# Optimization experiments

Measured on AMD Instinct MI355X. Metric: run time of the kernel, lower is better.

## Reference

```python
import jax, jax.numpy as jnp
import numpy as np

DIM = 768
HEADS = 12
HEAD_DIM = 64
INNER = HEADS * HEAD_DIM  # 768


def setup_inputs() -> dict:
    key = jax.random.key(0)
    k_x, k_wqkv, k_bqkv, k_wout, k_bout = jax.random.split(key, 5)
    B, S = 2, 2048
    x = jax.random.normal(k_x, (B, S, DIM), dtype=jnp.float32)
    # nn.Linear(dim, 3*inner): weight [out, in]; store transposed for x @ W
    lim = 1.0 / np.sqrt(DIM)
    w_qkv = jax.random.uniform(k_wqkv, (DIM, 3 * INNER), minval=-lim, maxval=lim, dtype=jnp.float32)
    b_qkv = jax.random.uniform(k_bqkv, (3 * INNER,), minval=-lim, maxval=lim, dtype=jnp.float32)
    lim2 = 1.0 / np.sqrt(INNER)
    # original zero-inits to_out; use random weights so the reference output is non-trivial
    w_out = jax.random.uniform(k_wout, (INNER, DIM), minval=-lim2, maxval=lim2, dtype=jnp.float32)
    b_out = jax.random.uniform(k_bout, (DIM,), minval=-lim2, maxval=lim2, dtype=jnp.float32)
    return {"x": x, "w_qkv": w_qkv, "b_qkv": b_qkv, "w_out": w_out, "b_out": b_out}


def reference(x, w_qkv, b_qkv, w_out, b_out):
    B, S, _ = x.shape
    qkv = x @ w_qkv + b_qkv                               # [B, S, 3*H*D]
    qkv = qkv.reshape(B, S, 3, HEADS, HEAD_DIM)           # b s three h d
    q, k, v = qkv[:, :, 0], qkv[:, :, 1], qkv[:, :, 2]    # each [B, S, H, D]
    scale = 1.0 / np.sqrt(HEAD_DIM)
    # non-causal self-attention (FlashSelfAttention, dropout=0, causal=False)
    scores = jnp.einsum('bshd,bthd->bhst', q, k) * scale  # [B, H, S, S]
    attn = jax.nn.softmax(scores, axis=-1)
    ctx = jnp.einsum('bhst,bthd->bshd', attn, v)          # [B, S, H, D]
    ctx = ctx.reshape(B, S, INNER)
    return ctx @ w_out + b_out                            # [B, S, DIM]
```

## Files before the change

kernel.cpp:

```cpp
#include <hip/hip_runtime.h>
#include <cstddef>
#include <cstdint>

#define DIM  768
#define NH   12
#define HD   64
#define SEQ  2048
#define NB   2
#define NQKV 2304
#define G    (NB * NH * SEQ)

typedef _Float16 f16x8 __attribute__((ext_vector_type(8)));
typedef _Float16 f16x4 __attribute__((ext_vector_type(4)));
typedef float    f32x4 __attribute__((ext_vector_type(4)));
typedef float    f32x16 __attribute__((ext_vector_type(16)));

#if __has_builtin(__builtin_amdgcn_exp2f)
#define EXP2(x) __builtin_amdgcn_exp2f(x)
#else
#define EXP2(x) exp2f(x)
#endif

#define QSCALE 0.1803368801111244f
#define C2     6.0f

__device__ __forceinline__ void gld16(const _Float16* g, _Float16* l) {
  __builtin_amdgcn_global_load_lds(
      (const __attribute__((address_space(1))) void*)g,
      (__attribute__((address_space(3))) void*)l, 16, 0, 0);
}

__global__ __launch_bounds__(256) void cvt_f16_kernel(
    const float* __restrict__ in, _Float16* __restrict__ out) {
  const size_t i = ((size_t)blockIdx.x * 256 + threadIdx.x) * 8;
  float4 f0 = *(const float4*)(in + i), f1 = *(const float4*)(in + i + 4);
  f16x8 o;
  o[0] = (_Float16)f0.x; o[1] = (_Float16)f0.y; o[2] = (_Float16)f0.z; o[3] = (_Float16)f0.w;
  o[4] = (_Float16)f1.x; o[5] = (_Float16)f1.y; o[6] = (_Float16)f1.z; o[7] = (_Float16)f1.w;
  *(f16x8*)(out + i) = o;
}

__global__ __launch_bounds__(256) void transpose_cvt_kernel(
    const float* __restrict__ W, _Float16* __restrict__ WT, int K, int N) {
  __shared__ _Float16 tl[32][36];
  const int t = threadIdx.x;
  const int k0 = blockIdx.y * 32, n0 = blockIdx.x * 32;
  {
    const int r = t >> 3, c4 = (t & 7) * 4;
    float4 f = *(const float4*)(W + (size_t)(k0 + r) * N + n0 + c4);
    tl[r][c4 + 0] = (_Float16)f.x; tl[r][c4 + 1] = (_Float16)f.y;
    tl[r][c4 + 2] = (_Float16)f.z; tl[r][c4 + 3] = (_Float16)f.w;
  }
  __syncthreads();
  const int n = t >> 3, kc = (t & 7) * 4;
  f16x4 v;
  v[0] = tl[kc + 0][n]; v[1] = tl[kc + 1][n];
  v[2] = tl[kc + 2][n]; v[3] = tl[kc + 3][n];
  *(f16x4*)(WT + (size_t)(n0 + n) * K + k0 + kc) = v;
}

__global__ __launch_bounds__(256) void vtrans_kernel(
    const _Float16* __restrict__ v, _Float16* __restrict__ vT) {
  __shared__ _Float16 tl[64][68];
  const int t = threadIdx.x;
  const int bh = blockIdx.x, st = blockIdx.y;
  const size_t base = (size_t)bh * SEQ * HD;
  {
    const int s = t >> 2, dc = (t & 3) * 16;
    const _Float16* p = v + base + (size_t)(st * 64 + s) * HD + dc;
    f16x8 a = *(const f16x8*)p, b = *(const f16x8*)(p + 8);
    *(f16x8*)&tl[s][dc] = a;
    *(f16x8*)&tl[s][dc + 8] = b;
  }
  __syncthreads();
  const int d = t >> 2, sc = (t & 3) * 16;
  f16x8 o0, o1;
#pragma unroll
  for (int j = 0; j < 8; j++) { o0[j] = tl[sc + j][d]; o1[j] = tl[sc + 8 + j][d]; }
  _Float16* q = vT + base + (size_t)d * SEQ + st * 64 + sc;
  *(f16x8*)q = o0;
  *(f16x8*)(q + 8) = o1;
}

template <int SC>
__global__ __launch_bounds__(256) void gemm_f16_kernel(
    const _Float16* __restrict__ A, const _Float16* __restrict__ BT,
    const float* __restrict__ bias, void* __restrict__ p0,
    void* __restrict__ p1, void* __restrict__ p2, int M, int N, int K) {
  __shared__ _Float16 As[128 * 32];
  __shared__ _Float16 Bs[128 * 32];
  const int tid = threadIdx.x;
  const int lane = tid & 63, wv = tid >> 6;
  const int wm = wv >> 1, wn = wv & 1;
  const int quad = lane >> 4, lcol = lane & 15;
  const int bm = blockIdx.y * 128, bn = blockIdx.x * 128;

  f32x4 acc[4][4];
#pragma unroll
  for (int i = 0; i < 4; i++)
#pragma unroll
    for (int j = 0; j < 4; j++) acc[i][j] = (f32x4)(0.f);

  const int r0 = wv * 32 + (lane >> 2);
  const int kp = (((lane & 3) ^ ((r0 >> 1) & 3)) * 8);
  const _Float16* a0p = A + (size_t)(bm + r0) * K + kp;
  const _Float16* a1p = A + (size_t)(bm + r0 + 16) * K + kp;
  const _Float16* b0p = BT + (size_t)(bn + r0) * K + kp;
  const _Float16* b1p = BT + (size_t)(bn + r0 + 16) * K + kp;
  _Float16* lA0 = As + (wv * 2 + 0) * 512;
  _Float16* lA1 = As + (wv * 2 + 1) * 512;
  _Float16* lB0 = Bs + (wv * 2 + 0) * 512;
  _Float16* lB1 = Bs + (wv * 2 + 1) * 512;

  for (int k0 = 0; k0 < K; k0 += 32) {
    __syncthreads();
    gld16(a0p + k0, lA0);
    gld16(a1p + k0, lA1);
    gld16(b0p + k0, lB0);
    gld16(b1p + k0, lB1);
    __syncthreads();

    f16x8 af[4], bf[4];
#pragma unroll
    for (int mi = 0; mi < 4; mi++) {
      const int R = wm * 64 + mi * 16 + lcol;
      af[mi] = *(const f16x8*)&As[R * 32 + (quad ^ ((R >> 1) & 3)) * 8];
    }
#pragma unroll
    for (int ni = 0; ni < 4; ni++) {
      const int R = wn * 64 + ni * 16 + lcol;
      bf[ni] = *(const f16x8*)&Bs[R * 32 + (quad ^ ((R >> 1) & 3)) * 8];
    }
#pragma unroll
    for (int mi = 0; mi < 4; mi++)
#pragma unroll
      for (int ni = 0; ni < 4; ni++)
        acc[mi][ni] = __builtin_amdgcn_mfma_f32_16x16x32_f16(af[mi], bf[ni], acc[mi][ni], 0, 0, 0);
  }

#pragma unroll
  for (int mi = 0; mi < 4; mi++) {
#pragma unroll
    for (int r = 0; r < 4; r++) {
      const int row = bm + wm * 64 + mi * 16 + quad * 4 + r;
      const int b_ = row >> 11, s_ = row & 2047;
#pragma unroll
      for (int ni = 0; ni < 4; ni++) {
        const int c = bn + wn * 64 + ni * 16 + lcol;
        const float val = acc[mi][ni][r] + bias[c];
        if (!SC) {
          ((float*)p0)[(size_t)row * N + c] = val;
        } else {
          const int d = c & 63;
          const int which = c / 768;
          const int h = (c - which * 768) >> 6;
          const size_t idx = (((size_t)b_ * NH + h) * SEQ + s_) * HD + d;
          if (which == 0)      ((_Float16*)p0)[idx] = (_Float16)(val * QSCALE);
          else if (which == 1) ((_Float16*)p1)[idx] = (_Float16)val;
          else                 ((_Float16*)p2)[idx] = (_Float16)val;
        }
      }
    }
  }
}

#define PST 68
__global__ __launch_bounds__(256) void attn_part_kernel(
    const _Float16* __restrict__ Q, const _Float16* __restrict__ K,
    const _Float16* __restrict__ V, _Float16* __restrict__ Ohat,
    float* __restrict__ L) {
  __shared__ _Float16 Ks[64 * PST];
  __shared__ _Float16 Vs[64 * PST];
  __shared__ _Float16 Ps[128 * PST];
  const int tid = threadIdx.x, lane = tid & 63, wv = tid >> 6;
  const int lr = lane & 31, hw = lane >> 5;
  const int bh = blockIdx.x, qt = blockIdx.y, ks = blockIdx.z;
  const size_t base = (size_t)bh * SEQ * HD;

  f16x8 qb[4];
  {
    const _Float16* qp = Q + base + (size_t)(qt * 128 + wv * 32 + lr) * HD + hw * 8;
#pragma unroll
    for (int f = 0; f < 4; f++) qb[f] = *(const f16x8*)(qp + f * 16);
  }

  f32x16 o0 = (f32x16)(0.f), o1 = (f32x16)(0.f);
  float l_part = 0.f;

  const int sr = tid >> 2;
  const int sc = (tid & 3) * 16;
  const _Float16* Kb = K + base + (size_t)ks * (SEQ / 2) * HD;
  const _Float16* Vb = V + base + ks * (SEQ / 2);

  for (int t = 0; t < (SEQ / 2) / 64; t++) {
    const _Float16* kp = Kb + (size_t)(t * 64 + sr) * HD + sc;
    f16x8 k0v = *(const f16x8*)kp, k1v = *(const f16x8*)(kp + 8);
    const _Float16* vp = Vb + (size_t)sr * SEQ + t * 64 + sc;
    f16x8 v0v = *(const f16x8*)vp, v1v = *(const f16x8*)(vp + 8);

    __syncthreads();
    *(f16x8*)&Ks[sr * PST + sc] = k0v;
    *(f16x8*)&Ks[sr * PST + sc + 8] = k1v;
    *(f16x8*)&Vs[sr * PST + sc] = v0v;
    *(f16x8*)&Vs[sr * PST + sc + 8] = v1v;
    __syncthreads();

    f32x16 s0 = (f32x16)(0.f), s1 = (f32x16)(0.f);
#pragma unroll
    for (int f = 0; f < 4; f++) {
      f16x8 ka0 = *(const f16x8*)&Ks[(lr) * PST + f * 16 + hw * 8];
      f16x8 ka1 = *(const f16x8*)&Ks[(32 + lr) * PST + f * 16 + hw * 8];
      s0 = __builtin_amdgcn_mfma_f32_32x32x16_f16(ka0, qb[f], s0, 0, 0, 0);
      s1 = __builtin_amdgcn_mfma_f32_32x32x16_f16(ka1, qb[f], s1, 0, 0, 0);
    }

    _Float16* pw = &Ps[(size_t)(wv * 32 + lr) * PST];
#pragma unroll
    for (int rg = 0; rg < 4; rg++) {
      f16x4 pk0, pk1;
#pragma unroll
      for (int i = 0; i < 4; i++) {
        const float p0 = EXP2(s0[rg * 4 + i] - C2);
        const float p1 = EXP2(s1[rg * 4 + i] - C2);
        l_part += p0 + p1;
        pk0[i] = (_Float16)p0;
        pk1[i] = (_Float16)p1;
      }
      *(f16x4*)&pw[0  + 8 * rg + 4 * hw] = pk0;
      *(f16x4*)&pw[32 + 8 * rg + 4 * hw] = pk1;
    }

#pragma unroll
    for (int f = 0; f < 4; f++) {
      f16x8 pa  = *(const f16x8*)&Ps[(size_t)(wv * 32 + lr) * PST + f * 16 + hw * 8];
      f16x8 vb0 = *(const f16x8*)&Vs[(lr) * PST + f * 16 + hw * 8];
      f16x8 vb1 = *(const f16x8*)&Vs[(32 + lr) * PST + f * 16 + hw * 8];
      o0 = __builtin_amdgcn_mfma_f32_32x32x16_f16(pa, vb0, o0, 0, 0, 0);
      o1 = __builtin_amdgcn_mfma_f32_32x32x16_f16(pa, vb1, o1, 0, 0, 0);
    }
  }

  const float l_full = l_part + __shfl_xor(l_part, 32);
  __syncthreads();
  float* lsh = (float*)&Ps[(size_t)(wv * 32) * PST];
  if (hw == 0) lsh[lr] = l_full;
  __syncthreads();

  const size_t rbase = (size_t)ks * G + (size_t)bh * SEQ + qt * 128 + wv * 32;
  if (hw == 0) L[rbase + lr] = l_full;
  float linv[16];
#pragma unroll
  for (int r = 0; r < 16; r++)
    linv[r] = 1.0f / lsh[(r & 3) + 8 * (r >> 2) + 4 * hw];
#pragma unroll
  for (int r = 0; r < 16; r++) {
    const int rr = (r & 3) + 8 * (r >> 2) + 4 * hw;
    _Float16* cp = Ohat + (rbase + rr) * HD;
    cp[lr]      = (_Float16)(o0[r] * linv[r]);
    cp[32 + lr] = (_Float16)(o1[r] * linv[r]);
  }
}

__global__ __launch_bounds__(256) void attn_merge_kernel(
    const _Float16* __restrict__ Ohat, const float* __restrict__ L,
    _Float16* __restrict__ ctx) {
  const size_t gid = (size_t)blockIdx.x * 256 + threadIdx.x;
  const int row = (int)(gid >> 3);
  const int dp = ((int)gid & 7) * 8;
  const float l0 = L[row], l1 = L[G + row];
  const float w0 = l0 / (l0 + l1), w1 = 1.0f - w0;
  f16x8 a = *(const f16x8*)(Ohat + (size_t)row * HD + dp);
  f16x8 b = *(const f16x8*)(Ohat + ((size_t)G + row) * HD + dp);
  const int bh = row >> 11, s = row & 2047;
  const int b_ = bh / NH, h_ = bh % NH;
  f16x8 o;
#pragma unroll
  for (int j = 0; j < 8; j++)
    o[j] = (_Float16)(w0 * (float)a[j] + w1 * (float)b[j]);
  *(f16x8*)(ctx + ((size_t)b_ * SEQ + s) * DIM + h_ * HD + dp) = o;
}

extern "C" void kernel_launch(void* const* d_in, const int* in_sizes, int n_in,
                              void* d_out, int out_size, void* d_ws,
                              size_t ws_size, hipStream_t stream) {
  const float* x = (const float*)d_in[0];
  const float* w_qkv = (const float*)d_in[1];
  const float* b_qkv = (const float*)d_in[2];
  const float* w_out = (const float*)d_in[3];
  const float* b_out = (const float*)d_in[4];
  float* out = (float*)d_out;

  _Float16* wsh = (_Float16*)d_ws;
  size_t off = 0;
  const size_t hsz = (size_t)NB * NH * SEQ * HD;
  _Float16* wqkvT = wsh + off; off += (size_t)NQKV * DIM;
  _Float16* woutT = wsh + off; off += (size_t)DIM * DIM;
  _Float16* qh   = wsh + off; off += hsz;
  _Float16* kh   = wsh + off; off += hsz;
  _Float16* vT   = wsh + off; off += hsz;
  _Float16* ctxh = wsh + off; off += hsz;
  _Float16* xh   = wsh + off; off += hsz;
  _Float16* vh   = wsh + off; off += hsz;
  float*    Lbuf = (float*)(wsh + off); off += 2 * (size_t)G * sizeof(float) / 2;
  _Float16* Ohat = xh;

  cvt_f16_kernel<<<(NB * SEQ * DIM) / (256 * 8), 256, 0, stream>>>(x, xh);
  transpose_cvt_kernel<<<dim3(NQKV / 32, DIM / 32), 256, 0, stream>>>(w_qkv, wqkvT, DIM, NQKV);
  transpose_cvt_kernel<<<dim3(DIM / 32, DIM / 32), 256, 0, stream>>>(w_out, woutT, DIM, DIM);
  gemm_f16_kernel<1><<<dim3(NQKV / 128, (NB * SEQ) / 128), 256, 0, stream>>>(
      xh, wqkvT, b_qkv, qh, kh, vh, NB * SEQ, NQKV, DIM);
  vtrans_kernel<<<dim3(NB * NH, SEQ / 64), 256, 0, stream>>>(vh, vT);
  attn_part_kernel<<<dim3(NB * NH, SEQ / 128, 2), 256, 0, stream>>>(
      qh, kh, vT, Ohat, Lbuf);
  attn_merge_kernel<<<(G * HD) / (256 * 8), 256, 0, stream>>>(Ohat, Lbuf, ctxh);
  gemm_f16_kernel<0><<<dim3(DIM / 128, (NB * SEQ) / 128), 256, 0, stream>>>(
      ctxh, woutT, b_out, out, nullptr, nullptr, NB * SEQ, DIM, DIM);
}
```

Measured before the change: 181.4 us.

## Fuse input conversion and V transpose into QKV GEMM; load V directly in attention

The QKV GEMM now reads fp32 x and converts it to f16 while staging into LDS, which removes the separate conversion kernel. It also writes V in transposed layout from its epilogue, which eliminates the vtrans kernel. GEMM K-tiles grow to 64 with an 8-way XOR swizzle, and the attention kernel loads V fragments straight from global memory into registers instead of staging them through LDS. The fixed exp offset is removed, which risks fp16 overflow in P for large scores.

```diff
diff --git a/kernel.cpp b/kernel.cpp
--- a/kernel.cpp
+++ b/kernel.cpp
@@ -22,22 +22,11 @@
 #endif
 
 #define QSCALE 0.1803368801111244f
-#define C2     6.0f
 
 __device__ __forceinline__ void gld16(const _Float16* g, _Float16* l) {
   __builtin_amdgcn_global_load_lds(
       (const __attribute__((address_space(1))) void*)g,
       (__attribute__((address_space(3))) void*)l, 16, 0, 0);
-}
-
-__global__ __launch_bounds__(256) void cvt_f16_kernel(
-    const float* __restrict__ in, _Float16* __restrict__ out) {
-  const size_t i = ((size_t)blockIdx.x * 256 + threadIdx.x) * 8;
-  float4 f0 = *(const float4*)(in + i), f1 = *(const float4*)(in + i + 4);
-  f16x8 o;
-  o[0] = (_Float16)f0.x; o[1] = (_Float16)f0.y; o[2] = (_Float16)f0.z; o[3] = (_Float16)f0.w;
-  o[4] = (_Float16)f1.x; o[5] = (_Float16)f1.y; o[6] = (_Float16)f1.z; o[7] = (_Float16)f1.w;
-  *(f16x8*)(out + i) = o;
 }
 
 __global__ __launch_bounds__(256) void transpose_cvt_kernel(
@@ -59,36 +48,13 @@
   *(f16x4*)(WT + (size_t)(n0 + n) * K + k0 + kc) = v;
 }
 
-__global__ __launch_bounds__(256) void vtrans_kernel(
-    const _Float16* __restrict__ v, _Float16* __restrict__ vT) {
-  __shared__ _Float16 tl[64][68];
-  const int t = threadIdx.x;
-  const int bh = blockIdx.x, st = blockIdx.y;
-  const size_t base = (size_t)bh * SEQ * HD;
-  {
-    const int s = t >> 2, dc = (t & 3) * 16;
-    const _Float16* p = v + base + (size_t)(st * 64 + s) * HD + dc;
-    f16x8 a = *(const f16x8*)p, b = *(const f16x8*)(p + 8);
-    *(f16x8*)&tl[s][dc] = a;
-    *(f16x8*)&tl[s][dc + 8] = b;
-  }
-  __syncthreads();
-  const int d = t >> 2, sc = (t & 3) * 16;
-  f16x8 o0, o1;
-#pragma unroll
-  for (int j = 0; j < 8; j++) { o0[j] = tl[sc + j][d]; o1[j] = tl[sc + 8 + j][d]; }
-  _Float16* q = vT + base + (size_t)d * SEQ + st * 64 + sc;
-  *(f16x8*)q = o0;
-  *(f16x8*)(q + 8) = o1;
-}
-
-template <int SC>
+template <int QKV>
 __global__ __launch_bounds__(256) void gemm_f16_kernel(
-    const _Float16* __restrict__ A, const _Float16* __restrict__ BT,
+    const void* __restrict__ Ap, const _Float16* __restrict__ BT,
     const float* __restrict__ bias, void* __restrict__ p0,
     void* __restrict__ p1, void* __restrict__ p2, int M, int N, int K) {
-  __shared__ _Float16 As[128 * 32];
-  __shared__ _Float16 Bs[128 * 32];
+  __shared__ _Float16 As[128 * 64];
+  __shared__ _Float16 Bs[128 * 64];
   const int tid = threadIdx.x;
   const int lane = tid & 63, wv = tid >> 6;
   const int wm = wv >> 1, wn = wv & 1;
@@ -101,41 +67,81 @@
 #pragma unroll
     for (int j = 0; j < 4; j++) acc[i][j] = (f32x4)(0.f);
 
-  const int r0 = wv * 32 + (lane >> 2);
-  const int kp = (((lane & 3) ^ ((r0 >> 1) & 3)) * 8);
-  const _Float16* a0p = A + (size_t)(bm + r0) * K + kp;
-  const _Float16* a1p = A + (size_t)(bm + r0 + 16) * K + kp;
-  const _Float16* b0p = BT + (size_t)(bn + r0) * K + kp;
-  const _Float16* b1p = BT + (size_t)(bn + r0 + 16) * K + kp;
-  _Float16* lA0 = As + (wv * 2 + 0) * 512;
-  _Float16* lA1 = As + (wv * 2 + 1) * 512;
-  _Float16* lB0 = Bs + (wv * 2 + 0) * 512;
-  _Float16* lB1 = Bs + (wv * 2 + 1) * 512;
-
-  for (int k0 = 0; k0 < K; k0 += 32) {
+  const _Float16* bsrc[4];
+  _Float16* bdst[4];
+  const _Float16* asrcH[4];
+  _Float16* adstH[4];
+#pragma unroll
+  for (int i = 0; i < 4; i++) {
+    const int r = 32 * i + 8 * wv + (lane >> 3);
+    const int c = lane & 7;
+    const int koff = ((c ^ (r & 7)) * 8);
+    bsrc[i] = BT + (size_t)(bn + r) * K + koff;
+    bdst[i] = Bs + (32 * i + 8 * wv) * 64;
+    if (!QKV) {
+      asrcH[i] = (const _Float16*)Ap + (size_t)(bm + r) * K + koff;
+      adstH[i] = As + (32 * i + 8 * wv) * 64;
+    }
+  }
+  const int rA = tid >> 1;
+  const float* asrcF[4];
+  _Float16* adstF[4];
+#pragma unroll
+  for (int w = 0; w < 4; w++) {
+    const int c = (tid & 1) * 4 + w;
+    asrcF[w] = (const float*)Ap + (size_t)(bm + rA) * K + c * 8;
+    adstF[w] = As + rA * 64 + ((c ^ (rA & 7)) * 8);
+  }
+
+  for (int k0 = 0; k0 < K; k0 += 64) {
+    float4 av0[4], av1[4];
+    if (QKV) {
+#pragma unroll
+      for (int w = 0; w < 4; w++) {
+        av0[w] = *(const float4*)(asrcF[w] + k0);
+        av1[w] = *(const float4*)(asrcF[w] + k0 + 4);
+      }
+    }
     __syncthreads();
-    gld16(a0p + k0, lA0);
-    gld16(a1p + k0, lA1);
-    gld16(b0p + k0, lB0);
-    gld16(b1p + k0, lB1);
+#pragma unroll
+    for (int i = 0; i < 4; i++) gld16(bsrc[i] + k0, bdst[i]);
+    if (!QKV) {
+#pragma unroll
+      for (int i = 0; i < 4; i++) gld16(asrcH[i] + k0, adstH[i]);
+    } else {
+#pragma unroll
+      for (int w = 0; w < 4; w++) {
+        f16x8 h;
+        h[0] = (_Float16)av0[w].x; h[1] = (_Float16)av0[w].y;
+        h[2] = (_Float16)av0[w].z; h[3] = (_Float16)av0[w].w;
+        h[4] = (_Float16)av1[w].x; h[5] = (_Float16)av1[w].y;
+        h[6] = (_Float16)av1[w].z; h[7] = (_Float16)av1[w].w;
+        *(f16x8*)adstF[w] = h;
+      }
+    }
     __syncthreads();
 
-    f16x8 af[4], bf[4];
-#pragma unroll
-    for (int mi = 0; mi < 4; mi++) {
-      const int R = wm * 64 + mi * 16 + lcol;
-      af[mi] = *(const f16x8*)&As[R * 32 + (quad ^ ((R >> 1) & 3)) * 8];
-    }
-#pragma unroll
-    for (int ni = 0; ni < 4; ni++) {
-      const int R = wn * 64 + ni * 16 + lcol;
-      bf[ni] = *(const f16x8*)&Bs[R * 32 + (quad ^ ((R >> 1) & 3)) * 8];
-    }
-#pragma unroll
-    for (int mi = 0; mi < 4; mi++)
-#pragma unroll
-      for (int ni = 0; ni < 4; ni++)
-        acc[mi][ni] = __builtin_amdgcn_mfma_f32_16x16x32_f16(af[mi], bf[ni], acc[mi][ni], 0, 0, 0);
+#pragma unroll
+    for (int kk = 0; kk < 2; kk++) {
+      f16x8 af[4], bf[4];
+#pragma unroll
+      for (int mi = 0; mi < 4; mi++) {
+        const int R = wm * 64 + mi * 16 + lcol;
+        const int q8 = kk * 4 + quad;
+        af[mi] = *(const f16x8*)&As[R * 64 + ((q8 ^ (R & 7)) * 8)];
+      }
+#pragma unroll
+      for (int ni = 0; ni < 4; ni++) {
+        const int R = wn * 64 + ni * 16 + lcol;
+        const int q8 = kk * 4 + quad;
+        bf[ni] = *(const f16x8*)&Bs[R * 64 + ((q8 ^ (R & 7)) * 8)];
+      }
+#pragma unroll
+      for (int mi = 0; mi < 4; mi++)
+#pragma unroll
+        for (int ni = 0; ni < 4; ni++)
+          acc[mi][ni] = __builtin_amdgcn_mfma_f32_16x16x32_f16(af[mi], bf[ni], acc[mi][ni], 0, 0, 0);
+    }
   }
 
 #pragma unroll
@@ -148,16 +154,19 @@
       for (int ni = 0; ni < 4; ni++) {
         const int c = bn + wn * 64 + ni * 16 + lcol;
         const float val = acc[mi][ni][r] + bias[c];
-        if (!SC) {
+        if (!QKV) {
           ((float*)p0)[(size_t)row * N + c] = val;
         } else {
           const int d = c & 63;
           const int which = c / 768;
           const int h = (c - which * 768) >> 6;
-          const size_t idx = (((size_t)b_ * NH + h) * SEQ + s_) * HD + d;
-          if (which == 0)      ((_Float16*)p0)[idx] = (_Float16)(val * QSCALE);
-          else if (which == 1) ((_Float16*)p1)[idx] = (_Float16)val;
-          else                 ((_Float16*)p2)[idx] = (_Float16)val;
+          if (which == 0)
+            ((_Float16*)p0)[(((size_t)b_ * NH + h) * SEQ + s_) * HD + d] =
+                (_Float16)(val * QSCALE);
+          else if (which == 1)
+            ((_Float16*)p1)[(((size_t)b_ * NH + h) * SEQ + s_) * HD + d] = (_Float16)val;
+          else
+            ((_Float16*)p2)[(((size_t)b_ * NH + h) * HD + d) * SEQ + s_] = (_Float16)val;
         }
       }
     }
@@ -170,7 +179,6 @@
     const _Float16* __restrict__ V, _Float16* __restrict__ Ohat,
     float* __restrict__ L) {
   __shared__ _Float16 Ks[64 * PST];
-  __shared__ _Float16 Vs[64 * PST];
   __shared__ _Float16 Ps[128 * PST];
   const int tid = threadIdx.x, lane = tid & 63, wv = tid >> 6;
   const int lr = lane & 31, hw = lane >> 5;
@@ -190,19 +198,24 @@
   const int sr = tid >> 2;
   const int sc = (tid & 3) * 16;
   const _Float16* Kb = K + base + (size_t)ks * (SEQ / 2) * HD;
-  const _Float16* Vb = V + base + ks * (SEQ / 2);
+  const _Float16* Vr0 = V + base + (size_t)lr * SEQ + ks * (SEQ / 2) + hw * 8;
+  const _Float16* Vr1 = V + base + (size_t)(32 + lr) * SEQ + ks * (SEQ / 2) + hw * 8;
+  _Float16* pw = &Ps[(size_t)(wv * 32 + lr) * PST];
+  const _Float16* pr = &Ps[(size_t)(wv * 32 + lr) * PST + hw * 8];
 
   for (int t = 0; t < (SEQ / 2) / 64; t++) {
     const _Float16* kp = Kb + (size_t)(t * 64 + sr) * HD + sc;
     f16x8 k0v = *(const f16x8*)kp, k1v = *(const f16x8*)(kp + 8);
-    const _Float16* vp = Vb + (size_t)sr * SEQ + t * 64 + sc;
-    f16x8 v0v = *(const f16x8*)vp, v1v = *(const f16x8*)(vp + 8);
+    f16x8 vbuf0[4], vbuf1[4];
+#pragma unroll
+    for (int f = 0; f < 4; f++) {
+      vbuf0[f] = *(const f16x8*)(Vr0 + t * 64 + f * 16);
+      vbuf1[f] = *(const f16x8*)(Vr1 + t * 64 + f * 16);
+    }
 
     __syncthreads();
     *(f16x8*)&Ks[sr * PST + sc] = k0v;
     *(f16x8*)&Ks[sr * PST + sc + 8] = k1v;
-    *(f16x8*)&Vs[sr * PST + sc] = v0v;
-    *(f16x8*)&Vs[sr * PST + sc + 8] = v1v;
     __syncthreads();
 
     f32x16 s0 = (f32x16)(0.f), s1 = (f32x16)(0.f);
@@ -214,14 +227,13 @@
       s1 = __builtin_amdgcn_mfma_f32_32x32x16_f16(ka1, qb[f], s1, 0, 0, 0);
     }
 
-    _Float16* pw = &Ps[(size_t)(wv * 32 + lr) * PST];
 #pragma unroll
     for (int rg = 0; rg < 4; rg++) {
       f16x4 pk0, pk1;
 #pragma unroll
       for (int i = 0; i < 4; i++) {
-        const float p0 = EXP2(s0[rg * 4 + i] - C2);
-        const float p1 = EXP2(s1[rg * 4 + i] - C2);
+        const float p0 = EXP2(s0[rg * 4 + i]);
+        const float p1 = EXP2(s1[rg * 4 + i]);
         l_part += p0 + p1;
         pk0[i] = (_Float16)p0;
         pk1[i] = (_Float16)p1;
@@ -232,11 +244,9 @@
 
 #pragma unroll
     for (int f = 0; f < 4; f++) {
-      f16x8 pa  = *(const f16x8*)&Ps[(size_t)(wv * 32 + lr) * PST + f * 16 + hw * 8];
-      f16x8 vb0 = *(const f16x8*)&Vs[(lr) * PST + f * 16 + hw * 8];
-      f16x8 vb1 = *(const f16x8*)&Vs[(32 + lr) * PST + f * 16 + hw * 8];
-      o0 = __builtin_amdgcn_mfma_f32_32x32x16_f16(pa, vb0, o0, 0, 0, 0);
-      o1 = __builtin_amdgcn_mfma_f32_32x32x16_f16(pa, vb1, o1, 0, 0, 0);
+      f16x8 pa = *(const f16x8*)(pr + f * 16);
+      o0 = __builtin_amdgcn_mfma_f32_32x32x16_f16(pa, vbuf0[f], o0, 0, 0, 0);
+      o1 = __builtin_amdgcn_mfma_f32_32x32x16_f16(pa, vbuf1[f], o1, 0, 0, 0);
     }
   }
 
@@ -299,17 +309,13 @@
   _Float16* kh   = wsh + off; off += hsz;
   _Float16* vT   = wsh + off; off += hsz;
   _Float16* ctxh = wsh + off; off += hsz;
-  _Float16* xh   = wsh + off; off += hsz;
-  _Float16* vh   = wsh + off; off += hsz;
-  float*    Lbuf = (float*)(wsh + off); off += 2 * (size_t)G * sizeof(float) / 2;
-  _Float16* Ohat = xh;
-
-  cvt_f16_kernel<<<(NB * SEQ * DIM) / (256 * 8), 256, 0, stream>>>(x, xh);
+  _Float16* Ohat = wsh + off; off += 2 * hsz;
+  float*    Lbuf = (float*)(wsh + off);
+
   transpose_cvt_kernel<<<dim3(NQKV / 32, DIM / 32), 256, 0, stream>>>(w_qkv, wqkvT, DIM, NQKV);
   transpose_cvt_kernel<<<dim3(DIM / 32, DIM / 32), 256, 0, stream>>>(w_out, woutT, DIM, DIM);
   gemm_f16_kernel<1><<<dim3(NQKV / 128, (NB * SEQ) / 128), 256, 0, stream>>>(
-      xh, wqkvT, b_qkv, qh, kh, vh, NB * SEQ, NQKV, DIM);
-  vtrans_kernel<<<dim3(NB * NH, SEQ / 64), 256, 0, stream>>>(vh, vT);
+      x, wqkvT, b_qkv, qh, kh, vT, NB * SEQ, NQKV, DIM);
   attn_part_kernel<<<dim3(NB * NH, SEQ / 128, 2), 256, 0, stream>>>(
       qh, kh, vT, Ohat, Lbuf);
   attn_merge_kernel<<<(G * HD) / (256 * 8), 256, 0, stream>>>(Ohat, Lbuf, ctxh);
```

New measurement: 220.5 us. 1.22x slower.

## Fuse x conversion into QKV GEMM and split-merge into output GEMM

Applied to the files above, without the earlier changes.

Removes the standalone fp32-to-fp16 conversion of x by loading fp32 x tiles directly in the QKV GEMM and converting them in registers before writing to LDS. Removes the attention merge kernel by having a new 64x64-tile output GEMM combine the two split-K partial outputs with their L weights while staging the A tile. The goal is to save two launches and the round trips of xh and ctx through global memory. In exchange, the A operand now goes through registers instead of async global-to-LDS loads, the merge weights are recomputed once per K-step, and the output GEMM uses smaller tiles without double buffering.

```diff
diff --git a/kernel.cpp b/kernel.cpp
--- a/kernel.cpp
+++ b/kernel.cpp
@@ -28,16 +28,6 @@
   __builtin_amdgcn_global_load_lds(
       (const __attribute__((address_space(1))) void*)g,
       (__attribute__((address_space(3))) void*)l, 16, 0, 0);
-}
-
-__global__ __launch_bounds__(256) void cvt_f16_kernel(
-    const float* __restrict__ in, _Float16* __restrict__ out) {
-  const size_t i = ((size_t)blockIdx.x * 256 + threadIdx.x) * 8;
-  float4 f0 = *(const float4*)(in + i), f1 = *(const float4*)(in + i + 4);
-  f16x8 o;
-  o[0] = (_Float16)f0.x; o[1] = (_Float16)f0.y; o[2] = (_Float16)f0.z; o[3] = (_Float16)f0.w;
-  o[4] = (_Float16)f1.x; o[5] = (_Float16)f1.y; o[6] = (_Float16)f1.z; o[7] = (_Float16)f1.w;
-  *(f16x8*)(out + i) = o;
 }
 
 __global__ __launch_bounds__(256) void transpose_cvt_kernel(
@@ -82,11 +72,10 @@
   *(f16x8*)(q + 8) = o1;
 }
 
-template <int SC>
-__global__ __launch_bounds__(256) void gemm_f16_kernel(
-    const _Float16* __restrict__ A, const _Float16* __restrict__ BT,
-    const float* __restrict__ bias, void* __restrict__ p0,
-    void* __restrict__ p1, void* __restrict__ p2, int M, int N, int K) {
+__global__ __launch_bounds__(256) void qkv_gemm_kernel(
+    const float* __restrict__ X, const _Float16* __restrict__ BT,
+    const float* __restrict__ bias, _Float16* __restrict__ q,
+    _Float16* __restrict__ k, _Float16* __restrict__ v) {
   __shared__ _Float16 As[128 * 32];
   __shared__ _Float16 Bs[128 * 32];
   const int tid = threadIdx.x;
@@ -94,6 +83,7 @@
   const int wm = wv >> 1, wn = wv & 1;
   const int quad = lane >> 4, lcol = lane & 15;
   const int bm = blockIdx.y * 128, bn = blockIdx.x * 128;
+  const int K = DIM, N = NQKV;
 
   f32x4 acc[4][4];
 #pragma unroll
@@ -101,35 +91,53 @@
 #pragma unroll
     for (int j = 0; j < 4; j++) acc[i][j] = (f32x4)(0.f);
 
+  const float* asrc[2];
+  _Float16* adst[2];
+#pragma unroll
+  for (int i = 0; i < 2; i++) {
+    const int rA = 64 * i + (tid >> 2);
+    const int cc = tid & 3;
+    asrc[i] = X + (size_t)(bm + rA) * K + cc * 8;
+    adst[i] = As + rA * 32 + ((cc ^ ((rA >> 1) & 3)) * 8);
+  }
   const int r0 = wv * 32 + (lane >> 2);
   const int kp = (((lane & 3) ^ ((r0 >> 1) & 3)) * 8);
-  const _Float16* a0p = A + (size_t)(bm + r0) * K + kp;
-  const _Float16* a1p = A + (size_t)(bm + r0 + 16) * K + kp;
   const _Float16* b0p = BT + (size_t)(bn + r0) * K + kp;
   const _Float16* b1p = BT + (size_t)(bn + r0 + 16) * K + kp;
-  _Float16* lA0 = As + (wv * 2 + 0) * 512;
-  _Float16* lA1 = As + (wv * 2 + 1) * 512;
   _Float16* lB0 = Bs + (wv * 2 + 0) * 512;
   _Float16* lB1 = Bs + (wv * 2 + 1) * 512;
 
   for (int k0 = 0; k0 < K; k0 += 32) {
-    __syncthreads();
-    gld16(a0p + k0, lA0);
-    gld16(a1p + k0, lA1);
+    float4 a0[2], a1[2];
+#pragma unroll
+    for (int i = 0; i < 2; i++) {
+      a0[i] = *(const float4*)(asrc[i] + k0);
+      a1[i] = *(const float4*)(asrc[i] + k0 + 4);
+    }
+    __syncthreads();
     gld16(b0p + k0, lB0);
     gld16(b1p + k0, lB1);
+#pragma unroll
+    for (int i = 0; i < 2; i++) {
+      f16x8 h;
+      h[0] = (_Float16)a0[i].x; h[1] = (_Float16)a0[i].y;
+      h[2] = (_Float16)a0[i].z; h[3] = (_Float16)a0[i].w;
+      h[4] = (_Float16)a1[i].x; h[5] = (_Float16)a1[i].y;
+      h[6] = (_Float16)a1[i].z; h[7] = (_Float16)a1[i].w;
+      *(f16x8*)adst[i] = h;
+    }
     __syncthreads();
 
     f16x8 af[4], bf[4];
 #pragma unroll
     for (int mi = 0; mi < 4; mi++) {
       const int R = wm * 64 + mi * 16 + lcol;
-      af[mi] = *(const f16x8*)&As[R * 32 + (quad ^ ((R >> 1) & 3)) * 8];
+      af[mi] = *(const f16x8*)&As[R * 32 + ((quad ^ ((R >> 1) & 3)) * 8)];
     }
 #pragma unroll
     for (int ni = 0; ni < 4; ni++) {
       const int R = wn * 64 + ni * 16 + lcol;
-      bf[ni] = *(const f16x8*)&Bs[R * 32 + (quad ^ ((R >> 1) & 3)) * 8];
+      bf[ni] = *(const f16x8*)&Bs[R * 32 + ((quad ^ ((R >> 1) & 3)) * 8)];
     }
 #pragma unroll
     for (int mi = 0; mi < 4; mi++)
@@ -148,17 +156,13 @@
       for (int ni = 0; ni < 4; ni++) {
         const int c = bn + wn * 64 + ni * 16 + lcol;
         const float val = acc[mi][ni][r] + bias[c];
-        if (!SC) {
-          ((float*)p0)[(size_t)row * N + c] = val;
-        } else {
-          const int d = c & 63;
-          const int which = c / 768;
-          const int h = (c - which * 768) >> 6;
-          const size_t idx = (((size_t)b_ * NH + h) * SEQ + s_) * HD + d;
-          if (which == 0)      ((_Float16*)p0)[idx] = (_Float16)(val * QSCALE);
-          else if (which == 1) ((_Float16*)p1)[idx] = (_Float16)val;
-          else                 ((_Float16*)p2)[idx] = (_Float16)val;
-        }
+        const int d = c & 63;
+        const int which = c / 768;
+        const int h = (c - which * 768) >> 6;
+        const size_t idx = (((size_t)b_ * NH + h) * SEQ + s_) * HD + d;
+        if (which == 0)      q[idx] = (_Float16)(val * QSCALE);
+        else if (which == 1) k[idx] = (_Float16)val;
+        else                 v[idx] = (_Float16)val;
       }
     }
   }
@@ -261,23 +265,71 @@
   }
 }
 
-__global__ __launch_bounds__(256) void attn_merge_kernel(
+__global__ __launch_bounds__(256) void out_gemm_kernel(
     const _Float16* __restrict__ Ohat, const float* __restrict__ L,
-    _Float16* __restrict__ ctx) {
-  const size_t gid = (size_t)blockIdx.x * 256 + threadIdx.x;
-  const int row = (int)(gid >> 3);
-  const int dp = ((int)gid & 7) * 8;
-  const float l0 = L[row], l1 = L[G + row];
-  const float w0 = l0 / (l0 + l1), w1 = 1.0f - w0;
-  f16x8 a = *(const f16x8*)(Ohat + (size_t)row * HD + dp);
-  f16x8 b = *(const f16x8*)(Ohat + ((size_t)G + row) * HD + dp);
-  const int bh = row >> 11, s = row & 2047;
-  const int b_ = bh / NH, h_ = bh % NH;
-  f16x8 o;
-#pragma unroll
-  for (int j = 0; j < 8; j++)
-    o[j] = (_Float16)(w0 * (float)a[j] + w1 * (float)b[j]);
-  *(f16x8*)(ctx + ((size_t)b_ * SEQ + s) * DIM + h_ * HD + dp) = o;
+    const _Float16* __restrict__ WT, const float* __restrict__ bias,
+    float* __restrict__ out) {
+  __shared__ _Float16 As[64 * 36];
+  __shared__ _Float16 Bs[64 * 36];
+  const int tid = threadIdx.x, lane = tid & 63, wv = tid >> 6;
+  const int wr = (wv >> 1) * 32, wc = (wv & 1) * 32;
+  const int quad = lane >> 4, lcol = lane & 15;
+  const int bm = blockIdx.y * 64, bn = blockIdx.x * 64;
+
+  f32x4 acc[2][2];
+#pragma unroll
+  for (int i = 0; i < 2; i++)
+#pragma unroll
+    for (int j = 0; j < 2; j++) acc[i][j] = (f32x4)(0.f);
+
+  const int ra = tid >> 2, ca = (tid & 3) * 8;
+  const int grow = bm + ra, b_ = grow >> 11, s_ = grow & 2047;
+
+  for (int k0 = 0; k0 < DIM; k0 += 32) {
+    const int h = k0 >> 6;
+    const int lidx = (b_ * NH + h) * SEQ + s_;
+    const size_t obase = (size_t)lidx * HD + (k0 & 32) + ca;
+    f16x8 u0 = *(const f16x8*)(Ohat + obase);
+    f16x8 u1 = *(const f16x8*)(Ohat + (size_t)G * HD + obase);
+    const float l0 = L[lidx], l1 = L[G + lidx];
+    const float w0 = l0 / (l0 + l1), w1 = 1.0f - w0;
+    f16x8 bv = *(const f16x8*)(WT + (size_t)(bn + ra) * DIM + k0 + ca);
+
+    __syncthreads();
+    f16x8 av;
+#pragma unroll
+    for (int j = 0; j < 8; j++)
+      av[j] = (_Float16)(w0 * (float)u0[j] + w1 * (float)u1[j]);
+    *(f16x8*)&As[ra * 36 + ca] = av;
+    *(f16x8*)&Bs[ra * 36 + ca] = bv;
+    __syncthreads();
+
+    f16x8 af[2], bf[2];
+#pragma unroll
+    for (int mi = 0; mi < 2; mi++)
+      af[mi] = *(const f16x8*)&As[(wr + mi * 16 + lcol) * 36 + quad * 8];
+#pragma unroll
+    for (int ni = 0; ni < 2; ni++)
+      bf[ni] = *(const f16x8*)&Bs[(wc + ni * 16 + lcol) * 36 + quad * 8];
+#pragma unroll
+    for (int mi = 0; mi < 2; mi++)
+#pragma unroll
+      for (int ni = 0; ni < 2; ni++)
+        acc[mi][ni] = __builtin_amdgcn_mfma_f32_16x16x32_f16(af[mi], bf[ni], acc[mi][ni], 0, 0, 0);
+  }
+
+#pragma unroll
+  for (int mi = 0; mi < 2; mi++) {
+#pragma unroll
+    for (int r = 0; r < 4; r++) {
+      const int row = bm + wr + mi * 16 + quad * 4 + r;
+#pragma unroll
+      for (int ni = 0; ni < 2; ni++) {
+        const int col = bn + wc + ni * 16 + lcol;
+        out[(size_t)row * DIM + col] = acc[mi][ni][r] + bias[col];
+      }
+    }
+  }
 }
 
 extern "C" void kernel_launch(void* const* d_in, const int* in_sizes, int n_in,
@@ -297,22 +349,18 @@
   _Float16* woutT = wsh + off; off += (size_t)DIM * DIM;
   _Float16* qh   = wsh + off; off += hsz;
   _Float16* kh   = wsh + off; off += hsz;
+  _Float16* vh   = wsh + off; off += hsz;
   _Float16* vT   = wsh + off; off += hsz;
-  _Float16* ctxh = wsh + off; off += hsz;
-  _Float16* xh   = wsh + off; off += hsz;
-  _Float16* vh   = wsh + off; off += hsz;
-  float*    Lbuf = (float*)(wsh + off); off += 2 * (size_t)G * sizeof(float) / 2;
-  _Float16* Ohat = xh;
-
-  cvt_f16_kernel<<<(NB * SEQ * DIM) / (256 * 8), 256, 0, stream>>>(x, xh);
+  _Float16* Ohat = wsh + off; off += 2 * hsz;
+  float*    Lbuf = (float*)(wsh + off);
+
   transpose_cvt_kernel<<<dim3(NQKV / 32, DIM / 32), 256, 0, stream>>>(w_qkv, wqkvT, DIM, NQKV);
   transpose_cvt_kernel<<<dim3(DIM / 32, DIM / 32), 256, 0, stream>>>(w_out, woutT, DIM, DIM);
-  gemm_f16_kernel<1><<<dim3(NQKV / 128, (NB * SEQ) / 128), 256, 0, stream>>>(
-      xh, wqkvT, b_qkv, qh, kh, vh, NB * SEQ, NQKV, DIM);
+  qkv_gemm_kernel<<<dim3(NQKV / 128, (NB * SEQ) / 128), 256, 0, stream>>>(
+      x, wqkvT, b_qkv, qh, kh, vh);
   vtrans_kernel<<<dim3(NB * NH, SEQ / 64), 256, 0, stream>>>(vh, vT);
   attn_part_kernel<<<dim3(NB * NH, SEQ / 128, 2), 256, 0, stream>>>(
       qh, kh, vT, Ohat, Lbuf);
-  attn_merge_kernel<<<(G * HD) / (256 * 8), 256, 0, stream>>>(Ohat, Lbuf, ctxh);
-  gemm_f16_kernel<0><<<dim3(DIM / 128, (NB * SEQ) / 128), 256, 0, stream>>>(
-      ctxh, woutT, b_out, out, nullptr, nullptr, NB * SEQ, DIM, DIM);
-}
+  out_gemm_kernel<<<dim3(DIM / 64, (NB * SEQ) / 64), 256, 0, stream>>>(
+      Ohat, Lbuf, woutT, b_out, out);
+}
```

Result: no change. 178.7 us (-1.5%).

## Double-buffer GEMM loads, fuse V transpose into QKV epilogue, retile output GEMM

Applied to the files above, without the earlier changes.

Both GEMMs now double-buffer their LDS tiles, so the next K-slice's global-to-LDS load is issued before the MFMAs on the current slice, with one waitcnt+barrier per iteration. The QKV GEMM writes V directly in transposed [b,h,d,s] layout, which removes the separate vtrans kernel and its round trip through memory. The output projection gets its own kernel with 64x64 tiles, giving more blocks (768 vs 192) for better CU occupancy. The transposed V store is strided per element, which may cost some write coalescing in the epilogue.

```diff
diff --git a/kernel.cpp b/kernel.cpp
--- a/kernel.cpp
+++ b/kernel.cpp
@@ -28,6 +28,10 @@
   __builtin_amdgcn_global_load_lds(
       (const __attribute__((address_space(1))) void*)g,
       (__attribute__((address_space(3))) void*)l, 16, 0, 0);
+}
+
+__device__ __forceinline__ void vm_barrier() {
+  asm volatile("s_waitcnt vmcnt(0)\ns_barrier" ::: "memory");
 }
 
 __global__ __launch_bounds__(256) void cvt_f16_kernel(
@@ -59,41 +63,18 @@
   *(f16x4*)(WT + (size_t)(n0 + n) * K + k0 + kc) = v;
 }
 
-__global__ __launch_bounds__(256) void vtrans_kernel(
-    const _Float16* __restrict__ v, _Float16* __restrict__ vT) {
-  __shared__ _Float16 tl[64][68];
-  const int t = threadIdx.x;
-  const int bh = blockIdx.x, st = blockIdx.y;
-  const size_t base = (size_t)bh * SEQ * HD;
-  {
-    const int s = t >> 2, dc = (t & 3) * 16;
-    const _Float16* p = v + base + (size_t)(st * 64 + s) * HD + dc;
-    f16x8 a = *(const f16x8*)p, b = *(const f16x8*)(p + 8);
-    *(f16x8*)&tl[s][dc] = a;
-    *(f16x8*)&tl[s][dc + 8] = b;
-  }
-  __syncthreads();
-  const int d = t >> 2, sc = (t & 3) * 16;
-  f16x8 o0, o1;
-#pragma unroll
-  for (int j = 0; j < 8; j++) { o0[j] = tl[sc + j][d]; o1[j] = tl[sc + 8 + j][d]; }
-  _Float16* q = vT + base + (size_t)d * SEQ + st * 64 + sc;
-  *(f16x8*)q = o0;
-  *(f16x8*)(q + 8) = o1;
-}
-
-template <int SC>
-__global__ __launch_bounds__(256) void gemm_f16_kernel(
-    const _Float16* __restrict__ A, const _Float16* __restrict__ BT,
-    const float* __restrict__ bias, void* __restrict__ p0,
-    void* __restrict__ p1, void* __restrict__ p2, int M, int N, int K) {
-  __shared__ _Float16 As[128 * 32];
-  __shared__ _Float16 Bs[128 * 32];
+__global__ __launch_bounds__(256) void qkv_gemm_kernel(
+    const _Float16* __restrict__ X, const _Float16* __restrict__ BT,
+    const float* __restrict__ bias, _Float16* __restrict__ q,
+    _Float16* __restrict__ k, _Float16* __restrict__ v) {
+  __shared__ _Float16 As[2][128 * 32];
+  __shared__ _Float16 Bs[2][128 * 32];
   const int tid = threadIdx.x;
   const int lane = tid & 63, wv = tid >> 6;
   const int wm = wv >> 1, wn = wv & 1;
   const int quad = lane >> 4, lcol = lane & 15;
   const int bm = blockIdx.y * 128, bn = blockIdx.x * 128;
+  const int K = DIM;
 
   f32x4 acc[4][4];
 #pragma unroll
@@ -103,39 +84,45 @@
 
   const int r0 = wv * 32 + (lane >> 2);
   const int kp = (((lane & 3) ^ ((r0 >> 1) & 3)) * 8);
-  const _Float16* a0p = A + (size_t)(bm + r0) * K + kp;
-  const _Float16* a1p = A + (size_t)(bm + r0 + 16) * K + kp;
+  const _Float16* a0p = X + (size_t)(bm + r0) * K + kp;
+  const _Float16* a1p = X + (size_t)(bm + r0 + 16) * K + kp;
   const _Float16* b0p = BT + (size_t)(bn + r0) * K + kp;
   const _Float16* b1p = BT + (size_t)(bn + r0 + 16) * K + kp;
-  _Float16* lA0 = As + (wv * 2 + 0) * 512;
-  _Float16* lA1 = As + (wv * 2 + 1) * 512;
-  _Float16* lB0 = Bs + (wv * 2 + 0) * 512;
-  _Float16* lB1 = Bs + (wv * 2 + 1) * 512;
-
-  for (int k0 = 0; k0 < K; k0 += 32) {
-    __syncthreads();
-    gld16(a0p + k0, lA0);
-    gld16(a1p + k0, lA1);
-    gld16(b0p + k0, lB0);
-    gld16(b1p + k0, lB1);
-    __syncthreads();
-
+  const int lo0 = (wv * 2 + 0) * 512;
+  const int lo1 = (wv * 2 + 1) * 512;
+
+  gld16(a0p, &As[0][lo0]);
+  gld16(a1p, &As[0][lo1]);
+  gld16(b0p, &Bs[0][lo0]);
+  gld16(b1p, &Bs[0][lo1]);
+  vm_barrier();
+
+  for (int t = 0; t < 24; t++) {
+    const int cur = t & 1, nxt = cur ^ 1;
+    if (t < 23) {
+      const int k1 = (t + 1) * 32;
+      gld16(a0p + k1, &As[nxt][lo0]);
+      gld16(a1p + k1, &As[nxt][lo1]);
+      gld16(b0p + k1, &Bs[nxt][lo0]);
+      gld16(b1p + k1, &Bs[nxt][lo1]);
+    }
     f16x8 af[4], bf[4];
 #pragma unroll
     for (int mi = 0; mi < 4; mi++) {
       const int R = wm * 64 + mi * 16 + lcol;
-      af[mi] = *(const f16x8*)&As[R * 32 + (quad ^ ((R >> 1) & 3)) * 8];
+      af[mi] = *(const f16x8*)&As[cur][R * 32 + ((quad ^ ((R >> 1) & 3)) * 8)];
     }
 #pragma unroll
     for (int ni = 0; ni < 4; ni++) {
       const int R = wn * 64 + ni * 16 + lcol;
-      bf[ni] = *(const f16x8*)&Bs[R * 32 + (quad ^ ((R >> 1) & 3)) * 8];
+      bf[ni] = *(const f16x8*)&Bs[cur][R * 32 + ((quad ^ ((R >> 1) & 3)) * 8)];
     }
 #pragma unroll
     for (int mi = 0; mi < 4; mi++)
 #pragma unroll
       for (int ni = 0; ni < 4; ni++)
         acc[mi][ni] = __builtin_amdgcn_mfma_f32_16x16x32_f16(af[mi], bf[ni], acc[mi][ni], 0, 0, 0);
+    vm_barrier();
   }
 
 #pragma unroll
@@ -148,17 +135,15 @@
       for (int ni = 0; ni < 4; ni++) {
         const int c = bn + wn * 64 + ni * 16 + lcol;
         const float val = acc[mi][ni][r] + bias[c];
-        if (!SC) {
-          ((float*)p0)[(size_t)row * N + c] = val;
-        } else {
-          const int d = c & 63;
-          const int which = c / 768;
-          const int h = (c - which * 768) >> 6;
-          const size_t idx = (((size_t)b_ * NH + h) * SEQ + s_) * HD + d;
-          if (which == 0)      ((_Float16*)p0)[idx] = (_Float16)(val * QSCALE);
-          else if (which == 1) ((_Float16*)p1)[idx] = (_Float16)val;
-          else                 ((_Float16*)p2)[idx] = (_Float16)val;
-        }
+        const int d = c & 63;
+        const int which = c / 768;
+        const int h = (c - which * 768) >> 6;
+        if (which == 0)
+          q[(((size_t)b_ * NH + h) * SEQ + s_) * HD + d] = (_Float16)(val * QSCALE);
+        else if (which == 1)
+          k[(((size_t)b_ * NH + h) * SEQ + s_) * HD + d] = (_Float16)val;
+        else
+          v[(((size_t)b_ * NH + h) * HD + d) * SEQ + s_] = (_Float16)val;
       }
     }
   }
@@ -280,6 +265,72 @@
   *(f16x8*)(ctx + ((size_t)b_ * SEQ + s) * DIM + h_ * HD + dp) = o;
 }
 
+__global__ __launch_bounds__(256) void out_gemm_kernel(
+    const _Float16* __restrict__ A, const _Float16* __restrict__ WT,
+    const float* __restrict__ bias, float* __restrict__ out) {
+  __shared__ _Float16 As[2][64 * 32];
+  __shared__ _Float16 Bs[2][64 * 32];
+  const int tid = threadIdx.x, lane = tid & 63, wv = tid >> 6;
+  const int wr = (wv >> 1) * 32, wc = (wv & 1) * 32;
+  const int quad = lane >> 4, lcol = lane & 15;
+  const int bm = blockIdx.y * 64, bn = blockIdx.x * 64;
+
+  f32x4 acc[2][2];
+#pragma unroll
+  for (int i = 0; i < 2; i++)
+#pragma unroll
+    for (int j = 0; j < 2; j++) acc[i][j] = (f32x4)(0.f);
+
+  const int r0 = wv * 16 + (lane >> 2);
+  const int kp = (((lane & 3) ^ ((r0 >> 1) & 3)) * 8);
+  const _Float16* asrc = A + (size_t)(bm + r0) * DIM + kp;
+  const _Float16* bsrc = WT + (size_t)(bn + r0) * DIM + kp;
+  const int lo = wv * 512;
+
+  gld16(asrc, &As[0][lo]);
+  gld16(bsrc, &Bs[0][lo]);
+  vm_barrier();
+
+  for (int t = 0; t < 24; t++) {
+    const int cur = t & 1, nxt = cur ^ 1;
+    if (t < 23) {
+      const int k1 = (t + 1) * 32;
+      gld16(asrc + k1, &As[nxt][lo]);
+      gld16(bsrc + k1, &Bs[nxt][lo]);
+    }
+    f16x8 af[2], bf[2];
+#pragma unroll
+    for (int mi = 0; mi < 2; mi++) {
+      const int R = wr + mi * 16 + lcol;
+      af[mi] = *(const f16x8*)&As[cur][R * 32 + ((quad ^ ((R >> 1) & 3)) * 8)];
+    }
+#pragma unroll
+    for (int ni = 0; ni < 2; ni++) {
+      const int R = wc + ni * 16 + lcol;
+      bf[ni] = *(const f16x8*)&Bs[cur][R * 32 + ((quad ^ ((R >> 1) & 3)) * 8)];
+    }
+#pragma unroll
+    for (int mi = 0; mi < 2; mi++)
+#pragma unroll
+      for (int ni = 0; ni < 2; ni++)
+        acc[mi][ni] = __builtin_amdgcn_mfma_f32_16x16x32_f16(af[mi], bf[ni], acc[mi][ni], 0, 0, 0);
+    vm_barrier();
+  }
+
+#pragma unroll
+  for (int mi = 0; mi < 2; mi++) {
+#pragma unroll
+    for (int r = 0; r < 4; r++) {
+      const int row = bm + wr + mi * 16 + quad * 4 + r;
+#pragma unroll
+      for (int ni = 0; ni < 2; ni++) {
+        const int col = bn + wc + ni * 16 + lcol;
+        out[(size_t)row * DIM + col] = acc[mi][ni][r] + bias[col];
+      }
+    }
+  }
+}
+
 extern "C" void kernel_launch(void* const* d_in, const int* in_sizes, int n_in,
                               void* d_out, int out_size, void* d_ws,
                               size_t ws_size, hipStream_t stream) {
@@ -295,24 +346,22 @@
   const size_t hsz = (size_t)NB * NH * SEQ * HD;
   _Float16* wqkvT = wsh + off; off += (size_t)NQKV * DIM;
   _Float16* woutT = wsh + off; off += (size_t)DIM * DIM;
+  _Float16* xh   = wsh + off; off += hsz;
   _Float16* qh   = wsh + off; off += hsz;
   _Float16* kh   = wsh + off; off += hsz;
   _Float16* vT   = wsh + off; off += hsz;
-  _Float16* ctxh = wsh + off; off += hsz;
-  _Float16* xh   = wsh + off; off += hsz;
-  _Float16* vh   = wsh + off; off += hsz;
-  float*    Lbuf = (float*)(wsh + off); off += 2 * (size_t)G * sizeof(float) / 2;
-  _Float16* Ohat = xh;
+  _Float16* Ohat = wsh + off; off += 2 * hsz;
+  float*    Lbuf = (float*)(wsh + off);
+  _Float16* ctxh = xh;
 
   cvt_f16_kernel<<<(NB * SEQ * DIM) / (256 * 8), 256, 0, stream>>>(x, xh);
   transpose_cvt_kernel<<<dim3(NQKV / 32, DIM / 32), 256, 0, stream>>>(w_qkv, wqkvT, DIM, NQKV);
   transpose_cvt_kernel<<<dim3(DIM / 32, DIM / 32), 256, 0, stream>>>(w_out, woutT, DIM, DIM);
-  gemm_f16_kernel<1><<<dim3(NQKV / 128, (NB * SEQ) / 128), 256, 0, stream>>>(
-      xh, wqkvT, b_qkv, qh, kh, vh, NB * SEQ, NQKV, DIM);
-  vtrans_kernel<<<dim3(NB * NH, SEQ / 64), 256, 0, stream>>>(vh, vT);
+  qkv_gemm_kernel<<<dim3(NQKV / 128, (NB * SEQ) / 128), 256, 0, stream>>>(
+      xh, wqkvT, b_qkv, qh, kh, vT);
   attn_part_kernel<<<dim3(NB * NH, SEQ / 128, 2), 256, 0, stream>>>(
       qh, kh, vT, Ohat, Lbuf);
   attn_merge_kernel<<<(G * HD) / (256 * 8), 256, 0, stream>>>(Ohat, Lbuf, ctxh);
-  gemm_f16_kernel<0><<<dim3(DIM / 128, (NB * SEQ) / 128), 256, 0, stream>>>(
-      ctxh, woutT, b_out, out, nullptr, nullptr, NB * SEQ, DIM, DIM);
-}
+  out_gemm_kernel<<<dim3(DIM / 64, (NB * SEQ) / 64), 256, 0, stream>>>(
+      ctxh, woutT, b_out, out);
+}
```

Result: no change. 184.2 us (+1.5%).
